# Optimization experiments

Hardware: AMD Instinct MI355X
Metric: run time of the kernel (lower is better)

Reference implementation:

```python
import jax, jax.numpy as jnp
import numpy as np

N, E, F, H, R, NB, G, C = 100000, 500000, 128, 64, 16, 30, 1000, 10


def setup_inputs() -> dict:
    key = jax.random.key(0)
    ks = jax.random.split(key, 12)
    s = 0.05
    x = jax.random.normal(ks[0], (N, F), jnp.float32)
    edge_index = jax.random.randint(ks[1], (2, E), 0, N, dtype=jnp.int32)
    edge_norm = jax.random.uniform(ks[2], (E,), jnp.float32)
    edge_type = jax.random.randint(ks[3], (E,), 0, R, dtype=jnp.int32)
    seq_lengths = jnp.full((G,), N // G, dtype=jnp.int32)  # 1000 graphs x 100 nodes
    return dict(
        x=x, edge_index=edge_index, edge_norm=edge_norm, edge_type=edge_type,
        seq_lengths=seq_lengths, avec=0,
        w1_rel=jax.random.normal(ks[4], (F, H), jnp.float32) * s,
        w1_root=jax.random.normal(ks[5], (F, H), jnp.float32) * s,
        b1=jnp.zeros((H,), jnp.float32),
        bases=jax.random.normal(ks[6], (NB, H, H), jnp.float32) * s,
        comp=jax.random.normal(ks[7], (R, NB), jnp.float32) * s,
        w2_root=jax.random.normal(ks[8], (H, H), jnp.float32) * s,
        b2=jnp.zeros((H,), jnp.float32),
        lin_w=jax.random.normal(ks[9], (2 * (F + H), H), jnp.float32) * s,
        lin_b=jnp.zeros((H,), jnp.float32),
        fc_w=jax.random.normal(ks[10], (H, C), jnp.float32) * s,
        fc_b=jnp.zeros((C,), jnp.float32),
    )


def reference(x, edge_index, edge_norm, edge_type, seq_lengths, avec,
              w1_rel, w1_root, b1, bases, comp, w2_root, b2,
              lin_w, lin_b, fc_w, fc_b):
    src, dst = edge_index[0], edge_index[1]

    # --- GraphConv (PyG): out_i = W_rel @ sum_{j->i} w_ji x_j + W_root x_i + b
    msg = x[src] * edge_norm[:, None]                       # [E, F]
    agg = jax.ops.segment_sum(msg, dst, num_segments=N)     # [N, F]
    h = agg @ w1_rel + x @ w1_root + b1                     # [N, H]

    # --- RGCNConv with basis decomposition, mean aggregation per relation
    W = jnp.einsum('rb,bio->rio', comp, bases)              # [R, H, H]
    hs = h[src]                                             # [E, H]
    out = h @ w2_root + b2                                  # root transform + bias
    for r in range(R):  # small fixed relation count
        m = (edge_type == r).astype(h.dtype)                # [E]
        s_r = jax.ops.segment_sum(hs * m[:, None], dst, num_segments=N)
        c_r = jax.ops.segment_sum(m, dst, num_segments=N)
        out = out + (s_r / jnp.maximum(c_r, 1.0)[:, None]) @ W[r]

    feats = jnp.concatenate([x, out], axis=-1)              # [N, F+H]

    # --- ragged per-graph sum & max pooling (replaces the Python loop)
    bounds = jnp.cumsum(seq_lengths)
    gid = jnp.searchsorted(bounds, jnp.arange(N), side='right')  # [N] graph ids
    gsum = jax.ops.segment_sum(feats, gid, num_segments=G)       # [G, F+H]
    gmax = jax.ops.segment_max(feats, gid, num_segments=G)       # [G, F+H]

    hidden = jax.nn.relu(jnp.concatenate([gsum, gmax], -1) @ lin_w + lin_b)
    # dropout is identity at inference
    logits = hidden @ fc_w + fc_b                           # [G, C]
    if avec:
        return logits
    return jax.nn.log_softmax(logits, -1)
```

## Files before the change

### kernel.cpp

```cpp
#include <hip/hip_runtime.h>
#include <hip/hip_bf16.h>

#define NN 100000
#define NE 500000
#define FD 128
#define HD 64
#define RR 16
#define NBASE 30
#define GG 1000
#define CC 10
#define NGROUP 6250


typedef __attribute__((ext_vector_type(8))) short bf16x8;
typedef __attribute__((ext_vector_type(4))) float f32x4;

__device__ inline unsigned short f2b(float x) {
  __hip_bfloat16 b = __float2bfloat16(x);
  return *reinterpret_cast<unsigned short*>(&b);
}
__device__ inline float b2f(unsigned short u) {
  return __uint_as_float(((unsigned)u) << 16);
}
__device__ inline unsigned pk2(float a, float b) {
  return (unsigned)f2b(a) | ((unsigned)f2b(b) << 16);
}

__global__ void k_basis(const float* comp, const float* bases, unsigned short* Wt) {
  int idx = blockIdx.x * 256 + threadIdx.x;
  int r = idx >> 12, kj = idx & 4095;
  int k = kj >> 6, n = kj & 63;
  float acc = 0.0f;
  for (int b = 0; b < NBASE; ++b)
    acc += comp[r * NBASE + b] * bases[b * 4096 + kj];
  int sk = (k & 15) * 4 + (k >> 4);
  Wt[(r << 12) + n * 64 + sk] = f2b(acc);
}

__global__ void k_wcvt(const float* w_root, const float* w_rel, const float* w2,
                       unsigned short* wcat, unsigned short* w2t) {
  int idx = blockIdx.x * 256 + threadIdx.x;
  if (idx < 16384) {
    int n = idx >> 7, k = idx & 127;
    float v = (n < 64) ? w_root[k * 64 + n] : w_rel[k * 64 + (n - 64)];
    wcat[n * 128 + k] = f2b(v);
  } else if (idx < 16384 + 4096) {
    int i2 = idx - 16384;
    int n = i2 >> 6, k = i2 & 63;
    int sk = (k & 15) * 4 + (k >> 4);
    w2t[n * 64 + sk] = f2b(w2[k * 64 + n]);
  }
}

__global__ __launch_bounds__(256) void k_proj_mfma(const float* x, const unsigned short* wcat,
                                                   const float* b1, unsigned short* hroot_bf,
                                                   unsigned short* xw_bf) {
  int wv = threadIdx.x >> 6, l = threadIdx.x & 63, m = l & 15, q = l >> 4;
  int gid = blockIdx.x * 4 + wv;
  int g = gid >> 1, half = gid & 1;
  if (g >= NGROUP) return;
  size_t n0 = (size_t)g * 16;
  const float* xr = x + (n0 + m) * FD + q * 8;
  float4 xv[8];
#pragma unroll
  for (int s = 0; s < 4; ++s) {
    xv[2 * s] = *reinterpret_cast<const float4*>(xr + s * 32);
    xv[2 * s + 1] = *reinterpret_cast<const float4*>(xr + s * 32 + 4);
  }
  f32x4 acc[4];
#pragma unroll
  for (int nt = 0; nt < 4; ++nt) acc[nt] = (f32x4){0, 0, 0, 0};
#pragma unroll
  for (int s = 0; s < 4; ++s) {
    float4 xa = xv[2 * s], xb = xv[2 * s + 1];
    bf16x8 a;
    a[0] = (short)f2b(xa.x); a[1] = (short)f2b(xa.y);
    a[2] = (short)f2b(xa.z); a[3] = (short)f2b(xa.w);
    a[4] = (short)f2b(xb.x); a[5] = (short)f2b(xb.y);
    a[6] = (short)f2b(xb.z); a[7] = (short)f2b(xb.w);
#pragma unroll
    for (int nt = 0; nt < 4; ++nt) {
      bf16x8 b = *reinterpret_cast<const bf16x8*>(
          wcat + ((half * 4 + nt) * 16 + m) * 128 + s * 32 + q * 8);
      acc[nt] = __builtin_amdgcn_mfma_f32_16x16x32_bf16(a, b, acc[nt], 0, 0, 0);
    }
  }
  float bv[4] = {0, 0, 0, 0};
  if (half == 0) {
#pragma unroll
    for (int nt = 0; nt < 4; ++nt) bv[nt] = b1[nt * 16 + m];
  }
  unsigned short* dbuf = half ? xw_bf : hroot_bf;
#pragma unroll
  for (int i = 0; i < 4; ++i) {
    size_t row = (n0 + q * 4 + i) * 64 + m * 4;
    uint2 o;
    o.x = pk2(acc[0][i] + bv[0], acc[1][i] + bv[1]);
    o.y = pk2(acc[2][i] + bv[2], acc[3][i] + bv[3]);
    *reinterpret_cast<uint2*>(dbuf + row) = o;
  }
}

__global__ void k_hists(const int* ei, const int* etype, int* hist1, int* hist2) {
  __shared__ int lh[RR];
  if (threadIdx.x < RR) lh[threadIdx.x] = 0;
  __syncthreads();
  for (int e = blockIdx.x * 256 + threadIdx.x; e < NE; e += gridDim.x * 256) {
    int t = etype[e];
    atomicAdd(&lh[t], 1);
    atomicAdd(&hist2[ei[NE + e] * RR + t], 1);
  }
  __syncthreads();
  if (threadIdx.x < RR) atomicAdd(&hist1[threadIdx.x], lh[threadIdx.x]);
}

__global__ void k_scan1(const int* hist1, int* offs, int* ctr1) {
  if (threadIdx.x == 0) {
    int s = 0;
    for (int r = 0; r < RR; ++r) { offs[r] = s; ctr1[r] = s; s += hist1[r]; }
    offs[RR] = s;
  }
}

__device__ inline int block_scan_incl(int v, int* ps, int t) {
  ps[t] = v;
  __syncthreads();
  for (int off = 1; off < 256; off <<= 1) {
    int u = (t >= off) ? ps[t - off] : 0;
    __syncthreads();
    ps[t] += u;
    __syncthreads();
  }
  return ps[t];
}

__global__ void k_scanA(const int* hist2, int* bsum) {
  __shared__ int red[256];
  int t = threadIdx.x;
  red[t] = hist2[blockIdx.x * 256 + t];
  __syncthreads();
  for (int s = 128; s; s >>= 1) {
    if (t < s) red[t] += red[t + s];
    __syncthreads();
  }
  if (t == 0) bsum[blockIdx.x] = red[0];
}

__global__ void k_scanB(int* bsum) {
  int t = threadIdx.x;
  int loc[25];
  int s = 0;
  if (t < 250) {
    for (int i = 0; i < 25; ++i) { loc[i] = bsum[t * 25 + i]; s += loc[i]; }
  }
  __shared__ int ps[256];
  int incl = block_scan_incl(s, ps, t);
  int base = incl - s;
  if (t < 250) {
    int run = base;
    for (int i = 0; i < 25; ++i) { int tmp = loc[i]; bsum[t * 25 + i] = run; run += tmp; }
  }
}

__global__ void k_scanC(const int* hist2, const int* bsum, int* rowptr2, int* ctr2) {
  int t = threadIdx.x;
  int gid = blockIdx.x * 256 + t;
  int v = hist2[gid];
  __shared__ int ps[256];
  int incl = block_scan_incl(v, ps, t);
  int ex = bsum[blockIdx.x] + incl - v;
  rowptr2[gid] = ex;
  ctr2[gid] = ex | (v << 20);
}

__global__ void k_sort(const int* ei, const int* etype, const float* enorm,
                       int* ctr1, int* ctr2, uint4* tse, uint2* esen) {
  __shared__ int lcnt[RR], lbase[RR];
  if (threadIdx.x < RR) lcnt[threadIdx.x] = 0;
  __syncthreads();
  int e = blockIdx.x * 256 + threadIdx.x;
  int t = 0, rank = 0;
  bool valid = e < NE;
  if (valid) { t = etype[e]; rank = atomicAdd(&lcnt[t], 1); }
  __syncthreads();
  if (threadIdx.x < RR) {
    int n = lcnt[threadIdx.x];
    lbase[threadIdx.x] = n ? atomicAdd(&ctr1[threadIdx.x], n) : 0;
  }
  __syncthreads();
  if (valid) {
    int p = lbase[t] + rank;
    int src = ei[e];
    int key = ei[NE + e] * RR + t;
    int old = atomicAdd(&ctr2[key], 1);
    int pos = old & 0xFFFFF;
    int cnt = old >> 20;
    float inv = 1.0f / (float)max(cnt, 1);
    float nrm = enorm[e];
    esen[pos] = make_uint2((unsigned)src, __float_as_uint(nrm));
    tse[p] = make_uint4((unsigned)src, __float_as_uint(inv), (unsigned)pos, 0u);
  }
}

__global__ __launch_bounds__(256) void k_gconv_seg(const int* rowptr2, const uint2* esen,
    const unsigned short* xw_bf, const unsigned short* hroot_bf, unsigned short* h_bf) {
  int wv = threadIdx.x >> 6, l = threadIdx.x & 63;
  int c4 = l & 15, eq = l >> 4;
  int dst = blockIdx.x * 4 + wv;
  int lo = rowptr2[dst * RR];
  int hi = (dst == NN - 1) ? NE : rowptr2[(dst + 1) * RR];
  float4 acc = {0.0f, 0.0f, 0.0f, 0.0f};
  for (int base0 = lo; base0 < hi; base0 += 64) {
    int n = min(64, hi - base0);
    int sv = 0;
    float nv = 0.0f;
    if (l < n) {
      uint2 se = esen[base0 + l];
      sv = (int)se.x;
      nv = __uint_as_float(se.y);
    }
    int k4max = (n + 3) >> 2;
    for (int k4 = 0; k4 < k4max; ++k4) {
      int eid = k4 * 4 + eq;
      int s = __shfl(sv, eid);
      float w = __shfl(nv, eid);
      if (eid < n) {
        uint2 v = *reinterpret_cast<const uint2*>(xw_bf + (size_t)s * 64 + c4 * 4);
        acc.x += b2f((unsigned short)(v.x & 0xffffu)) * w;
        acc.y += b2f((unsigned short)(v.x >> 16)) * w;
        acc.z += b2f((unsigned short)(v.y & 0xffffu)) * w;
        acc.w += b2f((unsigned short)(v.y >> 16)) * w;
      }
    }
  }
  acc.x += __shfl_xor(acc.x, 16); acc.y += __shfl_xor(acc.y, 16);
  acc.z += __shfl_xor(acc.z, 16); acc.w += __shfl_xor(acc.w, 16);
  acc.x += __shfl_xor(acc.x, 32); acc.y += __shfl_xor(acc.y, 32);
  acc.z += __shfl_xor(acc.z, 32); acc.w += __shfl_xor(acc.w, 32);
  if (l < 16) {
    uint2 hb = *reinterpret_cast<const uint2*>(hroot_bf + (size_t)dst * 64 + l * 4);
    acc.x += b2f((unsigned short)(hb.x & 0xffffu));
    acc.y += b2f((unsigned short)(hb.x >> 16));
    acc.z += b2f((unsigned short)(hb.y & 0xffffu));
    acc.w += b2f((unsigned short)(hb.y >> 16));
    uint2 o;
    o.x = pk2(acc.x, acc.y);
    o.y = pk2(acc.z, acc.w);
    *reinterpret_cast<uint2*>(h_bf + (size_t)dst * 64 + l * 4) = o;
  }
}

__global__ __launch_bounds__(256) void k_rgcn_y(const uint4* tse, const int* offs,
    const unsigned short* h_bf, const unsigned short* Wt, unsigned short* y_bf) {
  int r = blockIdx.x;
  int lo = offs[r], hi = offs[r + 1];
  int cnt = hi - lo;
  int wv = threadIdx.x >> 6;
  int l = threadIdx.x & 63;
  int m = l & 15, q = l >> 4;
  int ngroups = (cnt + 15) / 16;
  const unsigned short* Wr = Wt + (r << 12);
  bf16x8 bfr[2][4];
#pragma unroll
  for (int s = 0; s < 2; ++s)
#pragma unroll
    for (int nt = 0; nt < 4; ++nt)
      bfr[s][nt] = *reinterpret_cast<const bf16x8*>(Wr + (nt * 16 + m) * 64 + s * 32 + q * 8);

  for (int g = blockIdx.y * 4 + wv; g < ngroups; g += gridDim.y * 4) {
    int base = lo + g * 16;
    int ne = min(16, hi - base);
    int p = base + ((m < ne) ? m : 0);
    uint4 t4 = tse[p];
    int src = (int)t4.x;
    float inv = __uint_as_float(t4.y);
    int pos = (int)t4.z;
    f32x4 acc[4];
#pragma unroll
    for (int nt = 0; nt < 4; ++nt) acc[nt] = (f32x4){0, 0, 0, 0};
    const unsigned short* hrow = h_bf + (size_t)src * 64 + q * 8;
#pragma unroll
    for (int s = 0; s < 2; ++s) {
      bf16x8 afr = *reinterpret_cast<const bf16x8*>(hrow + s * 32);
#pragma unroll
      for (int nt = 0; nt < 4; ++nt)
        acc[nt] = __builtin_amdgcn_mfma_f32_16x16x32_bf16(afr, bfr[s][nt], acc[nt], 0, 0, 0);
    }
#pragma unroll
    for (int i = 0; i < 4; ++i) {
      int row = q * 4 + i;
      float ir = __shfl(inv, row);
      int pr = __shfl(pos, row);
      if (row < ne) {
        uint2 o;
        o.x = pk2(acc[0][i] * ir, acc[1][i] * ir);
        o.y = pk2(acc[2][i] * ir, acc[3][i] * ir);
        *reinterpret_cast<uint2*>(y_bf + (size_t)pr * 64 + m * 4) = o;
      }
    }
  }
}

__global__ __launch_bounds__(256) void k_out(const int* rowptr2, const unsigned short* y_bf,
    const unsigned short* h_bf, const unsigned short* w2t, const float* b2, float* out) {
  __shared__ float ldsC[16][68];
  int wv = threadIdx.x >> 6, l = threadIdx.x & 63;
  int c4 = l & 15, eq = l >> 4;
  size_t d0 = (size_t)blockIdx.x * 16;
  for (int dd = 0; dd < 4; ++dd) {
    int dst = (int)d0 + wv * 4 + dd;
    int lo = rowptr2[dst * RR];
    int hi = (dst == NN - 1) ? NE : rowptr2[(dst + 1) * RR];
    float4 acc = {0.0f, 0.0f, 0.0f, 0.0f};
    for (int row = lo + eq; row < hi; row += 4) {
      uint2 v = *reinterpret_cast<const uint2*>(y_bf + (size_t)row * 64 + c4 * 4);
      acc.x += b2f((unsigned short)(v.x & 0xffffu));
      acc.y += b2f((unsigned short)(v.x >> 16));
      acc.z += b2f((unsigned short)(v.y & 0xffffu));
      acc.w += b2f((unsigned short)(v.y >> 16));
    }
    acc.x += __shfl_xor(acc.x, 16); acc.y += __shfl_xor(acc.y, 16);
    acc.z += __shfl_xor(acc.z, 16); acc.w += __shfl_xor(acc.w, 16);
    acc.x += __shfl_xor(acc.x, 32); acc.y += __shfl_xor(acc.y, 32);
    acc.z += __shfl_xor(acc.z, 32); acc.w += __shfl_xor(acc.w, 32);
    if (l < 16)
      *reinterpret_cast<float4*>(&ldsC[wv * 4 + dd][l * 4]) = acc;
  }
  __syncthreads();
  int m = l & 15, q = l >> 4, nt = wv;
  float bb = b2[nt * 16 + m];
  f32x4 acc;
#pragma unroll
  for (int i = 0; i < 4; ++i) acc[i] = ldsC[q * 4 + i][m * 4 + nt] + bb;
#pragma unroll
  for (int s = 0; s < 2; ++s) {
    bf16x8 a = *reinterpret_cast<const bf16x8*>(h_bf + (d0 + m) * 64 + s * 32 + q * 8);
    bf16x8 b = *reinterpret_cast<const bf16x8*>(w2t + (nt * 16 + m) * 64 + s * 32 + q * 8);
    acc = __builtin_amdgcn_mfma_f32_16x16x32_bf16(a, b, acc, 0, 0, 0);
  }
#pragma unroll
  for (int i = 0; i < 4; ++i)
    out[(d0 + q * 4 + i) * 64 + nt * 16 + m] = acc[i];
}

__global__ void k_bounds(const int* seq, int* bounds) {
  __shared__ int s[GG];
  for (int i = threadIdx.x; i < GG; i += 256) s[i] = seq[i];
  __syncthreads();
  if (threadIdx.x == 0) {
    int acc = 0;
    for (int g = 0; g < GG; ++g) { acc += s[g]; bounds[g] = acc; }
  }
}

__global__ __launch_bounds__(256) void k_head(const float* x, const float* outn,
    const int* bounds, const float* lin_w, const float* lin_b,
    const float* fc_w, const float* fc_b, float* dout) {
  __shared__ float4 psum[5][48], pmax[5][48];
  __shared__ float gsum[192], gmax[192];
  __shared__ float part[4][64];
  __shared__ float hid[HD], lg[CC], mred[2];
  int g = blockIdx.x, t = threadIdx.x;
  int lo = (g == 0) ? 0 : bounds[g - 1];
  int hi = bounds[g];
  int nn = hi - lo;
  if (t < 240) {
    int c4 = t % 48, ch = t / 48;
    int a = lo + (nn * ch) / 5, b = lo + (nn * (ch + 1)) / 5;
    float4 s = {0, 0, 0, 0};
    float4 mx = {-3.4e38f, -3.4e38f, -3.4e38f, -3.4e38f};
    const float* bp;
    int stride;
    if (c4 < 32) { bp = x + (size_t)a * FD + c4 * 4; stride = FD; }
    else         { bp = outn + (size_t)a * 64 + (c4 - 32) * 4; stride = 64; }
    int n = a;
    for (; n + 4 <= b; n += 4) {
      float4 v0 = *reinterpret_cast<const float4*>(bp);
      float4 v1 = *reinterpret_cast<const float4*>(bp + stride);
      float4 v2 = *reinterpret_cast<const float4*>(bp + 2 * stride);
      float4 v3 = *reinterpret_cast<const float4*>(bp + 3 * stride);
      bp += 4 * stride;
      s.x += v0.x + v1.x + v2.x + v3.x;
      s.y += v0.y + v1.y + v2.y + v3.y;
      s.z += v0.z + v1.z + v2.z + v3.z;
      s.w += v0.w + v1.w + v2.w + v3.w;
      mx.x = fmaxf(fmaxf(fmaxf(mx.x, v0.x), fmaxf(v1.x, v2.x)), v3.x);
      mx.y = fmaxf(fmaxf(fmaxf(mx.y, v0.y), fmaxf(v1.y, v2.y)), v3.y);
      mx.z = fmaxf(fmaxf(fmaxf(mx.z, v0.z), fmaxf(v1.z, v2.z)), v3.z);
      mx.w = fmaxf(fmaxf(fmaxf(mx.w, v0.w), fmaxf(v1.w, v2.w)), v3.w);
    }
    for (; n < b; ++n) {
      float4 v = *reinterpret_cast<const float4*>(bp);
      bp += stride;
      s.x += v.x; s.y += v.y; s.z += v.z; s.w += v.w;
      mx.x = fmaxf(mx.x, v.x); mx.y = fmaxf(mx.y, v.y);
      mx.z = fmaxf(mx.z, v.z); mx.w = fmaxf(mx.w, v.w);
    }
    psum[ch][c4] = s;
    pmax[ch][c4] = mx;
  }
  __syncthreads();
  if (t < 48) {
    float4 s = psum[0][t], m = pmax[0][t];
#pragma unroll
    for (int ch = 1; ch < 5; ++ch) {
      float4 ps = psum[ch][t], pm = pmax[ch][t];
      s.x += ps.x; s.y += ps.y; s.z += ps.z; s.w += ps.w;
      m.x = fmaxf(m.x, pm.x); m.y = fmaxf(m.y, pm.y);
      m.z = fmaxf(m.z, pm.z); m.w = fmaxf(m.w, pm.w);
    }
    gsum[t * 4 + 0] = s.x; gsum[t * 4 + 1] = s.y;
    gsum[t * 4 + 2] = s.z; gsum[t * 4 + 3] = s.w;
    gmax[t * 4 + 0] = m.x; gmax[t * 4 + 1] = m.y;
    gmax[t * 4 + 2] = m.z; gmax[t * 4 + 3] = m.w;
  }
  __syncthreads();
  {
    int o = t & 63, pp = t >> 6;
    float a = 0.0f;
    int k0 = pp * 96;
    for (int k = k0; k < k0 + 96; ++k) {
      float gv = (k < 192) ? gsum[k] : gmax[k - 192];
      a += gv * lin_w[k * 64 + o];
    }
    part[pp][o] = a;
  }
  __syncthreads();
  if (t < HD) {
    float a = lin_b[t] + part[0][t] + part[1][t] + part[2][t] + part[3][t];
    hid[t] = fmaxf(a, 0.0f);
  }
  __syncthreads();
  if (t < CC) {
    float a = fc_b[t];
    for (int k = 0; k < HD; ++k) a += hid[k] * fc_w[k * CC + t];
    lg[t] = a;
  }
  __syncthreads();
  if (t == 0) {
    float mm = lg[0];
#pragma unroll
    for (int i = 1; i < CC; ++i) mm = fmaxf(mm, lg[i]);
    float se = 0.0f;
#pragma unroll
    for (int i = 0; i < CC; ++i) se += __expf(lg[i] - mm);
    mred[0] = mm;
    mred[1] = __logf(se);
  }
  __syncthreads();
  if (t < CC) dout[g * CC + t] = lg[t] - mred[0] - mred[1];
}

extern "C" void kernel_launch(void* const* d_in, const int* in_sizes, int n_in,
                              void* d_out, int out_size, void* d_ws, size_t ws_size,
                              hipStream_t stream) {
  const float* x     = (const float*)d_in[0];
  const int* ei      = (const int*)d_in[1];
  const float* enorm = (const float*)d_in[2];
  const int* etype   = (const int*)d_in[3];
  const int* seq     = (const int*)d_in[4];
  const float* w1_rel  = (const float*)d_in[6];
  const float* w1_root = (const float*)d_in[7];
  const float* b1      = (const float*)d_in[8];
  const float* bases   = (const float*)d_in[9];
  const float* comp    = (const float*)d_in[10];
  const float* w2      = (const float*)d_in[11];
  const float* b2      = (const float*)d_in[12];
  const float* lin_w   = (const float*)d_in[13];
  const float* lin_b   = (const float*)d_in[14];
  const float* fc_w    = (const float*)d_in[15];
  const float* fc_b    = (const float*)d_in[16];
  float* dout = (float*)d_out;

  char* p = (char*)d_ws;
  unsigned short* hroot_bf = (unsigned short*)p; p += (size_t)NN * 64 * 2;
  unsigned short* xw_bf    = (unsigned short*)p; p += (size_t)NN * 64 * 2;
  float* out  = (float*)p;  p += (size_t)NN * 64 * 4;
  unsigned short* y_bf = (unsigned short*)p; p += (size_t)NE * 64 * 2;
  unsigned short* h_bf = (unsigned short*)p; p += (size_t)NN * 64 * 2;
  unsigned short* Wt   = (unsigned short*)p; p += (size_t)RR * 4096 * 2;
  unsigned short* wcat = (unsigned short*)p; p += (size_t)128 * 128 * 2;
  unsigned short* w2t  = (unsigned short*)p; p += (size_t)64 * 64 * 2;
  uint4* tse   = (uint4*)p; p += (size_t)NE * 16;
  uint2* esen  = (uint2*)p; p += (size_t)NE * 8;
  int* hist2   = (int*)p; p += (size_t)NN * RR * 4;
  int* rowptr2 = (int*)p; p += (size_t)NN * RR * 4;
  int* bsum    = (int*)p; p += (size_t)NGROUP * 4;
  int* hist1   = (int*)p; p += 64;
  int* ctr1    = (int*)p; p += 64;
  int* offs    = (int*)p; p += 68;
  int* bounds  = (int*)p; p += (size_t)GG * 4;
  int* ctr2    = (int*)out;

  hipMemsetAsync(hist2, 0, (size_t)NN * RR * 4, stream);
  hipMemsetAsync(hist1, 0, 128, stream);

  hipLaunchKernelGGL(k_basis, dim3(256), dim3(256), 0, stream, comp, bases, Wt);
  hipLaunchKernelGGL(k_wcvt, dim3(80), dim3(256), 0, stream, w1_root, w1_rel, w2, wcat, w2t);
  hipLaunchKernelGGL(k_proj_mfma, dim3((2 * NGROUP + 3) / 4), dim3(256), 0, stream,
                     x, wcat, b1, hroot_bf, xw_bf);
  hipLaunchKernelGGL(k_hists, dim3(512), dim3(256), 0, stream, ei, etype, hist1, hist2);
  hipLaunchKernelGGL(k_scan1, dim3(1), dim3(64), 0, stream, hist1, offs, ctr1);
  hipLaunchKernelGGL(k_scanA, dim3(NGROUP), dim3(256), 0, stream, hist2, bsum);
  hipLaunchKernelGGL(k_scanB, dim3(1), dim3(256), 0, stream, bsum);
  hipLaunchKernelGGL(k_scanC, dim3(NGROUP), dim3(256), 0, stream, hist2, bsum, rowptr2, ctr2);
  hipLaunchKernelGGL(k_sort, dim3((NE + 255) / 256), dim3(256), 0, stream,
                     ei, etype, enorm, ctr1, ctr2, tse, esen);
  hipLaunchKernelGGL(k_gconv_seg, dim3(NN / 4), dim3(256), 0, stream,
                     rowptr2, esen, xw_bf, hroot_bf, h_bf);
  hipLaunchKernelGGL(k_rgcn_y, dim3(RR, 128), dim3(256), 0, stream,
                     tse, offs, h_bf, Wt, y_bf);
  hipLaunchKernelGGL(k_out, dim3(NN / 16), dim3(256), 0, stream,
                     rowptr2, y_bf, h_bf, w2t, b2, out);
  hipLaunchKernelGGL(k_bounds, dim3(1), dim3(256), 0, stream, seq, bounds);
  hipLaunchKernelGGL(k_head, dim3(GG), dim3(256), 0, stream, x, out, bounds,
                     lin_w, lin_b, fc_w, fc_b, dout);
}
```

Before: 371.8 us.

## Merge prep kernels and replace relation-count atomics with per-block scan

Merges the basis-combination and weight-conversion kernels into one launch. The per-relation counting sort now records per-block histograms, and a single-block scan kernel turns them into per-block bases, replacing the global atomic counters and the k_scan1 kernel. The same scan kernel computes graph bounds with a parallel scan, replacing the serial k_bounds kernel. This cuts kernel launches and global atomics, at the cost of a serial 1-block scan over about 1954 blocks × 16 relations.

Measured after the change: 360.0 us (median of 2 runs). 3.2% less time.

```diff
diff --git a/kernel.cpp b/kernel.cpp
--- a/kernel.cpp
+++ b/kernel.cpp
@@ -10,6 +10,7 @@
 #define GG 1000
 #define CC 10
 #define NGROUP 6250
+#define NBLK ((NE + 255) / 256)
 
 
 typedef __attribute__((ext_vector_type(8))) short bf16x8;
@@ -26,29 +27,31 @@
   return (unsigned)f2b(a) | ((unsigned)f2b(b) << 16);
 }
 
-__global__ void k_basis(const float* comp, const float* bases, unsigned short* Wt) {
-  int idx = blockIdx.x * 256 + threadIdx.x;
-  int r = idx >> 12, kj = idx & 4095;
-  int k = kj >> 6, n = kj & 63;
-  float acc = 0.0f;
-  for (int b = 0; b < NBASE; ++b)
-    acc += comp[r * NBASE + b] * bases[b * 4096 + kj];
-  int sk = (k & 15) * 4 + (k >> 4);
-  Wt[(r << 12) + n * 64 + sk] = f2b(acc);
-}
-
-__global__ void k_wcvt(const float* w_root, const float* w_rel, const float* w2,
+__global__ void k_prep(const float* comp, const float* bases, const float* w_root,
+                       const float* w_rel, const float* w2, unsigned short* Wt,
                        unsigned short* wcat, unsigned short* w2t) {
-  int idx = blockIdx.x * 256 + threadIdx.x;
-  if (idx < 16384) {
-    int n = idx >> 7, k = idx & 127;
-    float v = (n < 64) ? w_root[k * 64 + n] : w_rel[k * 64 + (n - 64)];
-    wcat[n * 128 + k] = f2b(v);
-  } else if (idx < 16384 + 4096) {
-    int i2 = idx - 16384;
-    int n = i2 >> 6, k = i2 & 63;
+  int bx = blockIdx.x;
+  if (bx < 256) {
+    int idx = bx * 256 + threadIdx.x;
+    int r = idx >> 12, kj = idx & 4095;
+    int k = kj >> 6, n = kj & 63;
+    float acc = 0.0f;
+    for (int b = 0; b < NBASE; ++b)
+      acc += comp[r * NBASE + b] * bases[b * 4096 + kj];
     int sk = (k & 15) * 4 + (k >> 4);
-    w2t[n * 64 + sk] = f2b(w2[k * 64 + n]);
+    Wt[(r << 12) + n * 64 + sk] = f2b(acc);
+  } else {
+    int idx = (bx - 256) * 256 + threadIdx.x;
+    if (idx < 16384) {
+      int n = idx >> 7, k = idx & 127;
+      float v = (n < 64) ? w_root[k * 64 + n] : w_rel[k * 64 + (n - 64)];
+      wcat[n * 128 + k] = f2b(v);
+    } else if (idx < 16384 + 4096) {
+      int i2 = idx - 16384;
+      int n = i2 >> 6, k = i2 & 63;
+      int sk = (k & 15) * 4 + (k >> 4);
+      w2t[n * 64 + sk] = f2b(w2[k * 64 + n]);
+    }
   }
 }
 
@@ -101,25 +104,18 @@
   }
 }
 
-__global__ void k_hists(const int* ei, const int* etype, int* hist1, int* hist2) {
+__global__ void k_hists(const int* ei, const int* etype, int* bch, int* hist2) {
   __shared__ int lh[RR];
   if (threadIdx.x < RR) lh[threadIdx.x] = 0;
   __syncthreads();
-  for (int e = blockIdx.x * 256 + threadIdx.x; e < NE; e += gridDim.x * 256) {
+  int e = blockIdx.x * 256 + threadIdx.x;
+  if (e < NE) {
     int t = etype[e];
     atomicAdd(&lh[t], 1);
     atomicAdd(&hist2[ei[NE + e] * RR + t], 1);
   }
   __syncthreads();
-  if (threadIdx.x < RR) atomicAdd(&hist1[threadIdx.x], lh[threadIdx.x]);
-}
-
-__global__ void k_scan1(const int* hist1, int* offs, int* ctr1) {
-  if (threadIdx.x == 0) {
-    int s = 0;
-    for (int r = 0; r < RR; ++r) { offs[r] = s; ctr1[r] = s; s += hist1[r]; }
-    offs[RR] = s;
-  }
+  if (threadIdx.x < RR) bch[blockIdx.x * RR + threadIdx.x] = lh[threadIdx.x];
 }
 
 __device__ inline int block_scan_incl(int v, int* ps, int t) {
@@ -173,33 +169,69 @@
   ctr2[gid] = ex | (v << 20);
 }
 
+__global__ void k_bscan(const int* bch, const int* seq, int* bbase, int* offs, int* bounds) {
+  __shared__ int part[16][17], chunkbase[16][17];
+  __shared__ int colbase[16];
+  __shared__ int ps[256];
+  int t = threadIdx.x;
+  int ty = t & 15, ck = t >> 4;
+  const int CH = (NBLK + 15) / 16;
+  int b0 = ck * CH, b1 = min(b0 + CH, NBLK);
+  int s = 0;
+  for (int b = b0; b < b1; ++b) s += bch[b * 16 + ty];
+  part[ck][ty] = s;
+  __syncthreads();
+  if (t < 16) {
+    int run = 0;
+    for (int c = 0; c < 16; ++c) { chunkbase[c][t] = run; run += part[c][t]; }
+    colbase[t] = run;
+  }
+  __syncthreads();
+  if (t == 0) {
+    int run = 0;
+    for (int r = 0; r < RR; ++r) { int v = colbase[r]; offs[r] = run; colbase[r] = run; run += v; }
+    offs[RR] = run;
+  }
+  __syncthreads();
+  {
+    int run = colbase[ty] + chunkbase[ck][ty];
+    for (int b = b0; b < b1; ++b) {
+      int v = bch[b * 16 + ty];
+      bbase[b * 16 + ty] = run;
+      run += v;
+    }
+  }
+  int loc[4];
+  int ss = 0;
+  if (t < 250) {
+    for (int i = 0; i < 4; ++i) { loc[i] = seq[t * 4 + i]; ss += loc[i]; }
+  }
+  int incl = block_scan_incl(ss, ps, t);
+  int base = incl - ss;
+  if (t < 250) {
+    int run = base;
+    for (int i = 0; i < 4; ++i) { run += loc[i]; bounds[t * 4 + i] = run; }
+  }
+}
+
 __global__ void k_sort(const int* ei, const int* etype, const float* enorm,
-                       int* ctr1, int* ctr2, uint4* tse, uint2* esen) {
-  __shared__ int lcnt[RR], lbase[RR];
+                       const int* bbase, int* ctr2, uint4* tse, uint2* esen) {
+  __shared__ int lcnt[RR];
   if (threadIdx.x < RR) lcnt[threadIdx.x] = 0;
   __syncthreads();
   int e = blockIdx.x * 256 + threadIdx.x;
-  int t = 0, rank = 0;
-  bool valid = e < NE;
-  if (valid) { t = etype[e]; rank = atomicAdd(&lcnt[t], 1); }
-  __syncthreads();
-  if (threadIdx.x < RR) {
-    int n = lcnt[threadIdx.x];
-    lbase[threadIdx.x] = n ? atomicAdd(&ctr1[threadIdx.x], n) : 0;
-  }
-  __syncthreads();
-  if (valid) {
-    int p = lbase[t] + rank;
-    int src = ei[e];
-    int key = ei[NE + e] * RR + t;
-    int old = atomicAdd(&ctr2[key], 1);
-    int pos = old & 0xFFFFF;
-    int cnt = old >> 20;
-    float inv = 1.0f / (float)max(cnt, 1);
-    float nrm = enorm[e];
-    esen[pos] = make_uint2((unsigned)src, __float_as_uint(nrm));
-    tse[p] = make_uint4((unsigned)src, __float_as_uint(inv), (unsigned)pos, 0u);
-  }
+  if (e >= NE) return;
+  int t = etype[e];
+  int rank = atomicAdd(&lcnt[t], 1);
+  int p = bbase[blockIdx.x * RR + t] + rank;
+  int src = ei[e];
+  int key = ei[NE + e] * RR + t;
+  int old = atomicAdd(&ctr2[key], 1);
+  int pos = old & 0xFFFFF;
+  int cnt = old >> 20;
+  float inv = 1.0f / (float)max(cnt, 1);
+  esen[pos] = make_uint2((unsigned)src, __float_as_uint(enorm[e]));
+  tse[p] = make_uint4((unsigned)src, __float_as_uint(inv), (unsigned)pos, 0u);
 }
 
 __global__ __launch_bounds__(256) void k_gconv_seg(const int* rowptr2, const uint2* esen,
@@ -341,16 +373,6 @@
 #pragma unroll
   for (int i = 0; i < 4; ++i)
     out[(d0 + q * 4 + i) * 64 + nt * 16 + m] = acc[i];
-}
-
-__global__ void k_bounds(const int* seq, int* bounds) {
-  __shared__ int s[GG];
-  for (int i = threadIdx.x; i < GG; i += 256) s[i] = seq[i];
-  __syncthreads();
-  if (threadIdx.x == 0) {
-    int acc = 0;
-    for (int g = 0; g < GG; ++g) { acc += s[g]; bounds[g] = acc; }
-  }
 }
 
 __global__ __launch_bounds__(256) void k_head(const float* x, const float* outn,
@@ -485,34 +507,32 @@
   uint2* esen  = (uint2*)p; p += (size_t)NE * 8;
   int* hist2   = (int*)p; p += (size_t)NN * RR * 4;
   int* rowptr2 = (int*)p; p += (size_t)NN * RR * 4;
+  int* bch     = (int*)p; p += (size_t)NBLK * RR * 4;
+  int* bbase   = (int*)p; p += (size_t)NBLK * RR * 4;
   int* bsum    = (int*)p; p += (size_t)NGROUP * 4;
-  int* hist1   = (int*)p; p += 64;
-  int* ctr1    = (int*)p; p += 64;
   int* offs    = (int*)p; p += 68;
   int* bounds  = (int*)p; p += (size_t)GG * 4;
   int* ctr2    = (int*)out;
 
   hipMemsetAsync(hist2, 0, (size_t)NN * RR * 4, stream);
-  hipMemsetAsync(hist1, 0, 128, stream);
-
-  hipLaunchKernelGGL(k_basis, dim3(256), dim3(256), 0, stream, comp, bases, Wt);
-  hipLaunchKernelGGL(k_wcvt, dim3(80), dim3(256), 0, stream, w1_root, w1_rel, w2, wcat, w2t);
+
+  hipLaunchKernelGGL(k_prep, dim3(256 + 80), dim3(256), 0, stream,
+                     comp, bases, w1_root, w1_rel, w2, Wt, wcat, w2t);
   hipLaunchKernelGGL(k_proj_mfma, dim3((2 * NGROUP + 3) / 4), dim3(256), 0, stream,
                      x, wcat, b1, hroot_bf, xw_bf);
-  hipLaunchKernelGGL(k_hists, dim3(512), dim3(256), 0, stream, ei, etype, hist1, hist2);
-  hipLaunchKernelGGL(k_scan1, dim3(1), dim3(64), 0, stream, hist1, offs, ctr1);
+  hipLaunchKernelGGL(k_hists, dim3(NBLK), dim3(256), 0, stream, ei, etype, bch, hist2);
   hipLaunchKernelGGL(k_scanA, dim3(NGROUP), dim3(256), 0, stream, hist2, bsum);
   hipLaunchKernelGGL(k_scanB, dim3(1), dim3(256), 0, stream, bsum);
   hipLaunchKernelGGL(k_scanC, dim3(NGROUP), dim3(256), 0, stream, hist2, bsum, rowptr2, ctr2);
-  hipLaunchKernelGGL(k_sort, dim3((NE + 255) / 256), dim3(256), 0, stream,
-                     ei, etype, enorm, ctr1, ctr2, tse, esen);
+  hipLaunchKernelGGL(k_bscan, dim3(1), dim3(256), 0, stream, bch, seq, bbase, offs, bounds);
+  hipLaunchKernelGGL(k_sort, dim3(NBLK), dim3(256), 0, stream,
+                     ei, etype, enorm, bbase, ctr2, tse, esen);
   hipLaunchKernelGGL(k_gconv_seg, dim3(NN / 4), dim3(256), 0, stream,
                      rowptr2, esen, xw_bf, hroot_bf, h_bf);
   hipLaunchKernelGGL(k_rgcn_y, dim3(RR, 128), dim3(256), 0, stream,
                      tse, offs, h_bf, Wt, y_bf);
   hipLaunchKernelGGL(k_out, dim3(NN / 16), dim3(256), 0, stream,
                      rowptr2, y_bf, h_bf, w2t, b2, out);
-  hipLaunchKernelGGL(k_bounds, dim3(1), dim3(256), 0, stream, seq, bounds);
   hipLaunchKernelGGL(k_head, dim3(GG), dim3(256), 0, stream, x, out, bounds,
                      lin_w, lin_b, fc_w, fc_b, dout);
 }
```
